# Optimization experiments

Hardware: AMD Instinct MI355X
Metric: run time of the kernel (lower is better)

Reference implementation:

```python
import jax, jax.numpy as jnp
import numpy as np

B, T, D, HS = 4, 2048, 1024, 64

def setup_inputs() -> dict:
    key = jax.random.key(0)
    kx, kk, kq, kv = jax.random.split(key, 4)
    scale = 1.0 / np.sqrt(D)
    return {
        "x": jax.random.normal(kx, (B, T, D), dtype=jnp.float32),
        "Wk": jax.random.normal(kk, (D, HS), dtype=jnp.float32) * scale,
        "Wq": jax.random.normal(kq, (D, HS), dtype=jnp.float32) * scale,
        "Wv": jax.random.normal(kv, (D, HS), dtype=jnp.float32) * scale,
    }

def reference(x, Wk, Wq, Wv):
    # x: [B, T, D]; projections to [B, T, HS]
    k = jnp.einsum("btd,dh->bth", x, Wk)
    q = jnp.einsum("btd,dh->bth", x, Wq)
    v = jnp.einsum("btd,dh->bth", x, Wv)
    # scores [B, T, T]; NOTE: original multiplies by sqrt(head_size) (faithful)
    att = jnp.einsum("bth,bsh->bts", q, k) * jnp.sqrt(jnp.float32(k.shape[-1]))
    Tq = x.shape[1]
    causal = jnp.tril(jnp.ones((Tq, Tq), dtype=bool))
    att = jnp.where(causal[None, :, :], att, -jnp.inf)
    p = jax.nn.softmax(att, axis=-1)
    # dropout = identity (eval mode)
    return jnp.einsum("bts,bsh->bth", p, v)
```

## Files before the change

kernel.cpp:

```cpp
#include <hip/hip_runtime.h>

#define Bn 4
#define Tn 2048
#define Dn 1024
#define HSn 64

typedef __attribute__((ext_vector_type(8))) short bf16x8;
typedef __attribute__((ext_vector_type(4))) float f32x4;
typedef __attribute__((ext_vector_type(4))) short s16x4;
typedef unsigned short u16;
typedef unsigned int u32;

__device__ __forceinline__ u16 f2bf_rne(float x) {
    u32 u = __float_as_uint(x);
    return (u16)((u + 0x7FFFu + ((u >> 16) & 1u)) >> 16);
}
__device__ __forceinline__ u16 f2bf_trunc(float x) {
    return (u16)(__float_as_uint(x) >> 16);
}
__device__ __forceinline__ float bf2f(u16 h) {
    return __uint_as_float(((u32)h) << 16);
}

#define GLL16(g, l)                                                        \
    __builtin_amdgcn_global_load_lds(                                      \
        (const __attribute__((address_space(1))) void*)(g),                \
        (__attribute__((address_space(3))) void*)(l), 16, 0, 0)

__global__ __launch_bounds__(256) void wprep_kernel(
    const float* __restrict__ Wk, const float* __restrict__ Wq,
    const float* __restrict__ Wv, u16* __restrict__ wtp)
{
    __shared__ float ws_[64][65];
    const int kb = blockIdx.x;
    const int w  = blockIdx.y;
    const float* __restrict__ W = (w == 0) ? Wk : (w == 1) ? Wq : Wv;
    const float scale = (w == 1) ? 8.0f : 1.0f;
    const int t = threadIdx.x;

    {
        const int kl = t >> 2, hq = t & 3;
        #pragma unroll
        for (int i = 0; i < 4; ++i) {
            float4 f = *(const float4*)(W + (size_t)(kb * 64 + kl) * 64 + hq * 16 + i * 4);
            ws_[kl][hq * 16 + i * 4 + 0] = f.x; ws_[kl][hq * 16 + i * 4 + 1] = f.y;
            ws_[kl][hq * 16 + i * 4 + 2] = f.z; ws_[kl][hq * 16 + i * 4 + 3] = f.w;
        }
    }
    __syncthreads();

    const int h = t & 63, quarter = t >> 6;
    const int n = w * 64 + h;
    const int ks = kb * 2 + (quarter >> 1);
    const int k_in0 = (quarter & 1) * 16;
    u16 hib[16], lob[16];
    #pragma unroll
    for (int j = 0; j < 16; ++j) {
        float v = ws_[quarter * 16 + j][h] * scale;
        u16 hi = f2bf_trunc(v);
        hib[j] = hi;
        lob[j] = f2bf_trunc(v - bf2f(hi));
    }
    u16* dst = wtp + (size_t)n * 2048 + ks * 64;
    *(uint4*)(dst + k_in0)          = *(const uint4*)&hib[0];
    *(uint4*)(dst + k_in0 + 8)      = *(const uint4*)&hib[8];
    *(uint4*)(dst + 32 + k_in0)     = *(const uint4*)&lob[0];
    *(uint4*)(dst + 32 + k_in0 + 8) = *(const uint4*)&lob[8];
}

#define NKS 32
#define XB(P) (smem + (P) * 4096)
#define BB(P) (smem + 12288 + (P) * 24576)

__global__ __launch_bounds__(512) void proj_gemm(
    const float* __restrict__ x, const u16* __restrict__ wtp,
    u16* __restrict__ qh8, u16* __restrict__ ql8,
    u16* __restrict__ kh,  u16* __restrict__ kl,
    u16* __restrict__ vt)
{
    __shared__ __align__(16) unsigned char smem[86016];

    const int tid  = threadIdx.x;
    const int wave = tid >> 6, lane = tid & 63;
    const int lo4  = lane & 15, g = lane >> 4;
    const int row0 = blockIdx.x * 32;
    const int rt   = wave >> 2;
    const int cbase = (wave & 3) * 3;
    const int rl = rt * 16 + lo4;

    f32x4 acc[3];
    #pragma unroll
    for (int c = 0; c < 3; ++c) acc[c] = (f32x4){0.f, 0.f, 0.f, 0.f};

    const int xr = (tid >> 3) & 31, xc = tid & 7;
    const int xsw = (xc ^ (xr & 7)) << 2;
    const float* xsrc0 = x + (size_t)(row0 + xr) * Dn + xsw;

    #define STAGE(P, KS)                                                     \
        {                                                                    \
            if (tid < 256) GLL16(xsrc0 + (KS) * 32, XB(P) + tid * 16);       \
            _Pragma("unroll")                                                \
            for (int i = 0; i < 3; ++i) {                                    \
                const int c = i * 512 + tid;                                 \
                const int n_ = c >> 3, p_ = c & 7;                           \
                const int l_ = p_ ^ (n_ & 7);                                \
                const u16* src = wtp + (size_t)n_ * 2048 + (KS) * 64         \
                                 + ((l_ & 3) << 3) + ((l_ >> 2) << 5);       \
                GLL16(src, BB(P) + c * 16);                                  \
            }                                                                \
        }

    #define COMPUTE(P, KS)                                                   \
        {                                                                    \
            bf16x8 ah, al;                                                   \
            {                                                                \
                const unsigned char* xb = XB(P) + rl * 128;                  \
                f32x4 f0 = *(const f32x4*)(xb + (((2 * g + 0) ^ (rl & 7)) << 4)); \
                f32x4 f1 = *(const f32x4*)(xb + (((2 * g + 1) ^ (rl & 7)) << 4)); \
                _Pragma("unroll")                                            \
                for (int jj = 0; jj < 4; ++jj) {                             \
                    u16 h0 = f2bf_trunc(f0[jj]);                             \
                    ah[jj] = (short)h0;                                      \
                    al[jj] = (short)f2bf_trunc(f0[jj] - bf2f(h0));           \
                    u16 h1 = f2bf_trunc(f1[jj]);                             \
                    ah[4 + jj] = (short)h1;                                  \
                    al[4 + jj] = (short)f2bf_trunc(f1[jj] - bf2f(h1));       \
                }                                                            \
            }                                                                \
            _Pragma("unroll")                                                \
            for (int ct = 0; ct < 3; ++ct) {                                 \
                const int n = (cbase + ct) * 16 + lo4;                       \
                const unsigned char* bb = BB(P) + n * 128;                   \
                bf16x8 bh = *(const bf16x8*)(bb + (((g)     ^ (n & 7)) << 4)); \
                bf16x8 bl = *(const bf16x8*)(bb + (((4 + g) ^ (n & 7)) << 4)); \
                acc[ct] = __builtin_amdgcn_mfma_f32_16x16x32_bf16(ah, bh, acc[ct], 0, 0, 0); \
                acc[ct] = __builtin_amdgcn_mfma_f32_16x16x32_bf16(al, bh, acc[ct], 0, 0, 0); \
                acc[ct] = __builtin_amdgcn_mfma_f32_16x16x32_bf16(ah, bl, acc[ct], 0, 0, 0); \
            }                                                                \
        }

    STAGE(0, 0)
    STAGE(1, 1)
    int pb = 0;
    for (int ks = 0; ks < NKS; ++ks) {
        if (ks == NKS - 1) {
            asm volatile("s_waitcnt vmcnt(0)" ::: "memory");
        } else if (wave < 4) {
            asm volatile("s_waitcnt vmcnt(4)" ::: "memory");
        } else {
            asm volatile("s_waitcnt vmcnt(3)" ::: "memory");
        }
        __builtin_amdgcn_s_barrier();
        asm volatile("" ::: "memory");

        int ps = pb + 2; if (ps >= 3) ps -= 3;
        if (ks + 2 < NKS) STAGE(ps, ks + 2)
        COMPUTE(pb, ks)
        pb = (pb == 2) ? 0 : pb + 1;
    }

    const int grow = row0 + rt * 16 + g * 4;
    #pragma unroll
    for (int ct = 0; ct < 3; ++ct) {
        const int n = (cbase + ct) * 16 + lo4;
        if (n < 64) {
            #pragma unroll
            for (int reg = 0; reg < 4; ++reg) {
                float v = acc[ct][reg];
                u16 hi = f2bf_trunc(v);
                kh[(size_t)(grow + reg) * HSn + n] = hi;
                kl[(size_t)(grow + reg) * HSn + n] = f2bf_trunc(v - bf2f(hi));
            }
        } else if (n < 128) {
            #pragma unroll
            for (int reg = 0; reg < 4; ++reg) {
                float v = acc[ct][reg];
                u16 hi = f2bf_trunc(v);
                qh8[(size_t)(grow + reg) * HSn + (n - 64)] = hi;
                ql8[(size_t)(grow + reg) * HSn + (n - 64)] = f2bf_trunc(v - bf2f(hi));
            }
        } else {
            s16x4 pack;
            #pragma unroll
            for (int reg = 0; reg < 4; ++reg)
                pack[reg] = (short)f2bf_rne(acc[ct][reg]);
            const int b = grow >> 11, tl = grow & 2047;
            *(s16x4*)(vt + ((size_t)b * HSn + (n - 128)) * Tn + tl) = pack;
        }
    }
}

struct KVset {
    bf16x8 kh0[2], kh1[2], kl0[2], kl1[2], vf[4];
};

__global__ __launch_bounds__(256, 2) void attn_kernel(
    const u16* __restrict__ qh8, const u16* __restrict__ ql8,
    const u16* __restrict__ kh, const u16* __restrict__ kl,
    const u16* __restrict__ vt, float* __restrict__ out)
{
    __shared__ __align__(16) unsigned char pbuf[4096];
    __shared__ __align__(16) float om_s[4][16][64];
    __shared__ float ml_s[4][16][2];

    const int tid  = threadIdx.x;
    const int wave = tid >> 6, lane = tid & 63;
    const int lo4  = lane & 15, g = lane >> 4;

    const int sblk = blockIdx.x >> 8, c = blockIdx.x & 255;
    const int tb = sblk ? 127 - (c >> 1) : (c >> 1);
    const int b  = 2 * sblk + (c & 1);
    const int t0 = tb * 16;

    const u16* qhp = qh8 + ((size_t)b * Tn + t0) * HSn;
    const u16* qlp = ql8 + ((size_t)b * Tn + t0) * HSn;
    const u16* khp = kh + (size_t)b * Tn * HSn;
    const u16* klp = kl + (size_t)b * Tn * HSn;
    const u16* vtp = vt + (size_t)b * HSn * Tn;

    bf16x8 qfh[2], qfl[2];
    #pragma unroll
    for (int ch = 0; ch < 2; ++ch) {
        qfh[ch] = *(const bf16x8*)(qhp + lo4 * HSn + ch * 32 + g * 8);
        qfl[ch] = *(const bf16x8*)(qlp + lo4 * HSn + ch * 32 + g * 8);
    }

    f32x4 O[4];
    #pragma unroll
    for (int n = 0; n < 4; ++n) O[n] = (f32x4){0.f, 0.f, 0.f, 0.f};
    float mrow[4], lrow[4];
    #pragma unroll
    for (int r = 0; r < 4; ++r) { mrow[r] = -1e30f; lrow[r] = 0.f; }

    const int nt = (t0 + 15) / 32 + 1;
    unsigned char* myPB = pbuf + wave * 1024;

    #define LOADSET(S, J)                                                     \
        {                                                                     \
            const int s0_ = (J) * 32;                                         \
            _Pragma("unroll")                                                 \
            for (int sb = 0; sb < 2; ++sb) {                                  \
                const u16* kr = khp + (size_t)(s0_ + sb * 16 + lo4) * HSn;    \
                const u16* lr = klp + (size_t)(s0_ + sb * 16 + lo4) * HSn;    \
                S.kh0[sb] = *(const bf16x8*)(kr + g * 8);                     \
                S.kh1[sb] = *(const bf16x8*)(kr + 32 + g * 8);                \
                S.kl0[sb] = *(const bf16x8*)(lr + g * 8);                     \
                S.kl1[sb] = *(const bf16x8*)(lr + 32 + g * 8);                \
            }                                                                 \
            _Pragma("unroll")                                                 \
            for (int n = 0; n < 4; ++n)                                       \
                S.vf[n] = *(const bf16x8*)(vtp + (size_t)(n * 16 + lo4) * Tn  \
                                           + s0_ + g * 8);                    \
        }

    #define COMPUTE_ATT(S, J)                                                 \
        {                                                                     \
            const int s0 = (J) * 32;                                          \
            f32x4 accS[2];                                                    \
            __builtin_amdgcn_s_setprio(1);                                    \
            _Pragma("unroll")                                                 \
            for (int sb = 0; sb < 2; ++sb) {                                  \
                f32x4 a = (f32x4){0.f, 0.f, 0.f, 0.f};                        \
                a = __builtin_amdgcn_mfma_f32_16x16x32_bf16(qfh[0], S.kh0[sb], a, 0, 0, 0); \
                a = __builtin_amdgcn_mfma_f32_16x16x32_bf16(qfh[1], S.kh1[sb], a, 0, 0, 0); \
                a = __builtin_amdgcn_mfma_f32_16x16x32_bf16(qfl[0], S.kh0[sb], a, 0, 0, 0); \
                a = __builtin_amdgcn_mfma_f32_16x16x32_bf16(qfl[1], S.kh1[sb], a, 0, 0, 0); \
                a = __builtin_amdgcn_mfma_f32_16x16x32_bf16(qfh[0], S.kl0[sb], a, 0, 0, 0); \
                a = __builtin_amdgcn_mfma_f32_16x16x32_bf16(qfh[1], S.kl1[sb], a, 0, 0, 0); \
                accS[sb] = a;                                                 \
            }                                                                 \
            __builtin_amdgcn_s_setprio(0);                                    \
            _Pragma("unroll")                                                 \
            for (int reg = 0; reg < 4; ++reg) {                               \
                const int tg  = t0 + g * 4 + reg;                             \
                const int sg0 = s0 + lo4;                                     \
                const int sg1 = s0 + 16 + lo4;                                \
                float v0 = (sg0 <= tg) ? accS[0][reg] : -1e30f;               \
                float v1 = (sg1 <= tg) ? accS[1][reg] : -1e30f;               \
                float mt = fmaxf(v0, v1);                                     \
                mt = fmaxf(mt, __shfl_xor(mt, 1));                            \
                mt = fmaxf(mt, __shfl_xor(mt, 2));                            \
                mt = fmaxf(mt, __shfl_xor(mt, 4));                            \
                mt = fmaxf(mt, __shfl_xor(mt, 8));                            \
                float mn = fmaxf(mrow[reg], mt);                              \
                float p0 = (sg0 <= tg) ? __expf(v0 - mn) : 0.f;               \
                float p1 = (sg1 <= tg) ? __expf(v1 - mn) : 0.f;               \
                float ps = p0 + p1;                                           \
                ps += __shfl_xor(ps, 1);                                      \
                ps += __shfl_xor(ps, 2);                                      \
                ps += __shfl_xor(ps, 4);                                      \
                ps += __shfl_xor(ps, 8);                                      \
                float alpha = __expf(mrow[reg] - mn);                         \
                lrow[reg] = lrow[reg] * alpha + ps;                           \
                mrow[reg] = mn;                                               \
                _Pragma("unroll")                                             \
                for (int n = 0; n < 4; ++n) O[n][reg] *= alpha;               \
                const int irow = g * 4 + reg;                                 \
                *(u16*)(myPB + ((irow * 64 + lo4 * 2) ^ (reg << 4)))      = f2bf_rne(p0); \
                *(u16*)(myPB + ((irow * 64 + 32 + lo4 * 2) ^ (reg << 4))) = f2bf_rne(p1); \
            }                                                                 \
            bf16x8 pf = *(const bf16x8*)(myPB + ((lo4 * 64 + 16 * g) ^ ((lo4 & 3) << 4))); \
            __builtin_amdgcn_s_setprio(1);                                    \
            _Pragma("unroll")                                                 \
            for (int n = 0; n < 4; ++n)                                       \
                O[n] = __builtin_amdgcn_mfma_f32_16x16x32_bf16(pf, S.vf[n], O[n], 0, 0, 0); \
            __builtin_amdgcn_s_setprio(0);                                    \
        }

    KVset A, B;
    int j = wave;
    if (j < nt) LOADSET(A, j)
    while (j < nt) {
        if (j + 4 < nt) LOADSET(B, j + 4)
        COMPUTE_ATT(A, j)
        if (j + 4 < nt) {
            if (j + 8 < nt) LOADSET(A, j + 8)
            COMPUTE_ATT(B, j + 4)
        }
        j += 8;
    }

    #pragma unroll
    for (int n = 0; n < 4; ++n)
        #pragma unroll
        for (int reg = 0; reg < 4; ++reg)
            om_s[wave][g * 4 + reg][n * 16 + lo4] = O[n][reg];
    if (lo4 == 0) {
        #pragma unroll
        for (int reg = 0; reg < 4; ++reg) {
            ml_s[wave][g * 4 + reg][0] = mrow[reg];
            ml_s[wave][g * 4 + reg][1] = lrow[reg];
        }
    }
    __syncthreads();

    const int r  = tid >> 4;
    const int h4 = (tid & 15) * 4;
    float mw[4], lw[4], mstar = -1e30f;
    #pragma unroll
    for (int w = 0; w < 4; ++w) {
        mw[w] = ml_s[w][r][0];
        lw[w] = ml_s[w][r][1];
        mstar = fmaxf(mstar, mw[w]);
    }
    float lstar = 0.f, ew[4];
    #pragma unroll
    for (int w = 0; w < 4; ++w) { ew[w] = __expf(mw[w] - mstar); lstar += lw[w] * ew[w]; }
    float4 a4 = {0.f, 0.f, 0.f, 0.f};
    #pragma unroll
    for (int w = 0; w < 4; ++w) {
        float4 t4 = *(const float4*)&om_s[w][r][h4];
        a4.x += t4.x * ew[w]; a4.y += t4.y * ew[w];
        a4.z += t4.z * ew[w]; a4.w += t4.w * ew[w];
    }
    const float inv = 1.f / lstar;
    a4.x *= inv; a4.y *= inv; a4.z *= inv; a4.w *= inv;
    *(float4*)(out + ((size_t)b * Tn + t0 + r) * HSn + h4) = a4;
}

extern "C" void kernel_launch(void* const* d_in, const int* in_sizes, int n_in,
                              void* d_out, int out_size, void* d_ws, size_t ws_size,
                              hipStream_t stream) {
    const float* x  = (const float*)d_in[0];
    const float* Wk = (const float*)d_in[1];
    const float* Wq = (const float*)d_in[2];
    const float* Wv = (const float*)d_in[3];
    float* out = (float*)d_out;

    const size_t per = (size_t)Bn * Tn * HSn;
    u16* qh8 = (u16*)d_ws;
    u16* ql8 = qh8 + per;
    u16* khw = ql8 + per;
    u16* klw = khw + per;
    u16* vtw = klw + per;
    u16* wtp = vtw + per;

    hipLaunchKernelGGL(wprep_kernel, dim3(16, 3), dim3(256), 0, stream,
                       Wk, Wq, Wv, wtp);
    hipLaunchKernelGGL(proj_gemm, dim3(256), dim3(512), 0, stream,
                       x, wtp, qh8, ql8, khw, klw, vtw);
    hipLaunchKernelGGL(attn_kernel, dim3(512), dim3(256), 0, stream,
                       qh8, ql8, khw, klw, vtw, out);
}
```

Baseline: 55.02 us.

## Store K and V in MFMA-fragment tiled layout for contiguous attention loads

The projection kernel now writes K hi/lo and V into a tiled layout that matches the per-lane MFMA fragment order, so each lane's 16-byte load in the attention kernel reads a contiguous 1KB span per wavefront. This replaces strided row loads (64-element or 2048-element strides) with fully coalesced loads and simplifies address arithmetic. The trade-off is that the projection epilogue now does scattered 2-byte stores for K, which may be less coalesced than before.

```diff
diff --git a/kernel.cpp b/kernel.cpp
--- a/kernel.cpp
+++ b/kernel.cpp
@@ -75,8 +75,8 @@
 __global__ __launch_bounds__(512) void proj_gemm(
     const float* __restrict__ x, const u16* __restrict__ wtp,
     u16* __restrict__ qh8, u16* __restrict__ ql8,
-    u16* __restrict__ kh,  u16* __restrict__ kl,
-    u16* __restrict__ vt)
+    u16* __restrict__ kth, u16* __restrict__ ktl,
+    u16* __restrict__ vtt)
 {
     __shared__ __align__(16) unsigned char smem[86016];
 
@@ -160,16 +160,20 @@
     }
 
     const int grow = row0 + rt * 16 + g * 4;
+    const int bb_ = grow >> 11, tl = grow & 2047;
     #pragma unroll
     for (int ct = 0; ct < 3; ++ct) {
         const int n = (cbase + ct) * 16 + lo4;
         if (n < 64) {
+            const int ch = n >> 5, gi = (n >> 3) & 3, e = n & 7;
+            const size_t base = (size_t)bb_ * 131072
+                + (size_t)(((((tl >> 4) * 2 + ch) * 4 + gi) * 16 + (tl & 15)) * 8 + e);
             #pragma unroll
             for (int reg = 0; reg < 4; ++reg) {
                 float v = acc[ct][reg];
                 u16 hi = f2bf_trunc(v);
-                kh[(size_t)(grow + reg) * HSn + n] = hi;
-                kl[(size_t)(grow + reg) * HSn + n] = f2bf_trunc(v - bf2f(hi));
+                kth[base + reg * 8] = hi;
+                ktl[base + reg * 8] = f2bf_trunc(v - bf2f(hi));
             }
         } else if (n < 128) {
             #pragma unroll
@@ -180,12 +184,15 @@
                 ql8[(size_t)(grow + reg) * HSn + (n - 64)] = f2bf_trunc(v - bf2f(hi));
             }
         } else {
+            const int h = n - 128;
             s16x4 pack;
             #pragma unroll
             for (int reg = 0; reg < 4; ++reg)
                 pack[reg] = (short)f2bf_rne(acc[ct][reg]);
-            const int b = grow >> 11, tl = grow & 2047;
-            *(s16x4*)(vt + ((size_t)b * HSn + (n - 128)) * Tn + tl) = pack;
+            const size_t vidx = (size_t)bb_ * 131072
+                + (size_t)((tl >> 5) * 2048 + (h >> 4) * 512 + (h & 15) * 32
+                           + ((tl >> 3) & 3) * 8 + (tl & 7));
+            *(s16x4*)(vtt + vidx) = pack;
         }
     }
 }
@@ -196,8 +203,8 @@
 
 __global__ __launch_bounds__(256, 2) void attn_kernel(
     const u16* __restrict__ qh8, const u16* __restrict__ ql8,
-    const u16* __restrict__ kh, const u16* __restrict__ kl,
-    const u16* __restrict__ vt, float* __restrict__ out)
+    const u16* __restrict__ kth, const u16* __restrict__ ktl,
+    const u16* __restrict__ vtt, float* __restrict__ out)
 {
     __shared__ __align__(16) unsigned char pbuf[4096];
     __shared__ __align__(16) float om_s[4][16][64];
@@ -214,9 +221,11 @@
 
     const u16* qhp = qh8 + ((size_t)b * Tn + t0) * HSn;
     const u16* qlp = ql8 + ((size_t)b * Tn + t0) * HSn;
-    const u16* khp = kh + (size_t)b * Tn * HSn;
-    const u16* klp = kl + (size_t)b * Tn * HSn;
-    const u16* vtp = vt + (size_t)b * HSn * Tn;
+    const u16* kthb = kth + (size_t)b * 131072;
+    const u16* ktlb = ktl + (size_t)b * 131072;
+    const u16* vttb = vtt + (size_t)b * 131072;
+    const int klane = lane * 8;
+    const int vlane = lo4 * 32 + g * 8;
 
     bf16x8 qfh[2], qfl[2];
     #pragma unroll
@@ -237,20 +246,21 @@
 
     #define LOADSET(S, J)                                                     \
         {                                                                     \
-            const int s0_ = (J) * 32;                                         \
-            _Pragma("unroll")                                                 \
-            for (int sb = 0; sb < 2; ++sb) {                                  \
-                const u16* kr = khp + (size_t)(s0_ + sb * 16 + lo4) * HSn;    \
-                const u16* lr = klp + (size_t)(s0_ + sb * 16 + lo4) * HSn;    \
-                S.kh0[sb] = *(const bf16x8*)(kr + g * 8);                     \
-                S.kh1[sb] = *(const bf16x8*)(kr + 32 + g * 8);                \
-                S.kl0[sb] = *(const bf16x8*)(lr + g * 8);                     \
-                S.kl1[sb] = *(const bf16x8*)(lr + 32 + g * 8);                \
-            }                                                                 \
-            _Pragma("unroll")                                                 \
-            for (int n = 0; n < 4; ++n)                                       \
-                S.vf[n] = *(const bf16x8*)(vtp + (size_t)(n * 16 + lo4) * Tn  \
-                                           + s0_ + g * 8);                    \
+            const u16* kb_ = kthb + (size_t)(2 * (J)) * 1024 + klane;         \
+            const u16* lb_ = ktlb + (size_t)(2 * (J)) * 1024 + klane;         \
+            S.kh0[0] = *(const bf16x8*)(kb_);                                 \
+            S.kh1[0] = *(const bf16x8*)(kb_ + 512);                           \
+            S.kh0[1] = *(const bf16x8*)(kb_ + 1024);                          \
+            S.kh1[1] = *(const bf16x8*)(kb_ + 1536);                          \
+            S.kl0[0] = *(const bf16x8*)(lb_);                                 \
+            S.kl1[0] = *(const bf16x8*)(lb_ + 512);                           \
+            S.kl0[1] = *(const bf16x8*)(lb_ + 1024);                          \
+            S.kl1[1] = *(const bf16x8*)(lb_ + 1536);                          \
+            const u16* vb_ = vttb + (size_t)(J) * 2048 + vlane;               \
+            S.vf[0] = *(const bf16x8*)(vb_);                                  \
+            S.vf[1] = *(const bf16x8*)(vb_ + 512);                            \
+            S.vf[2] = *(const bf16x8*)(vb_ + 1024);                           \
+            S.vf[3] = *(const bf16x8*)(vb_ + 1536);                           \
         }
 
     #define COMPUTE_ATT(S, J)                                                 \
@@ -370,15 +380,15 @@
     const size_t per = (size_t)Bn * Tn * HSn;
     u16* qh8 = (u16*)d_ws;
     u16* ql8 = qh8 + per;
-    u16* khw = ql8 + per;
-    u16* klw = khw + per;
-    u16* vtw = klw + per;
-    u16* wtp = vtw + per;
+    u16* kth = ql8 + per;
+    u16* ktl = kth + per;
+    u16* vtt = ktl + per;
+    u16* wtp = vtt + per;
 
     hipLaunchKernelGGL(wprep_kernel, dim3(16, 3), dim3(256), 0, stream,
                        Wk, Wq, Wv, wtp);
     hipLaunchKernelGGL(proj_gemm, dim3(256), dim3(512), 0, stream,
-                       x, wtp, qh8, ql8, khw, klw, vtw);
+                       x, wtp, qh8, ql8, kth, ktl, vtt);
     hipLaunchKernelGGL(attn_kernel, dim3(512), dim3(256), 0, stream,
-                       qh8, ql8, khw, klw, vtw, out);
-}
+                       qh8, ql8, kth, ktl, vtt, out);
+}
```

After: 49.48 us. 10.1% less time.
